# Kernel tuning notes

Hardware: AMD Instinct MI355X
Metric: run time of the kernel (lower is better)

Reference implementation:

```python
import jax, jax.numpy as jnp
import numpy as np

N = 100_000      # num_nodes
E = 1_600_000    # num directed edges (avg degree 16)
F_IN = 64
F_OUT = 64
ALPHA = 0.5      # args.alphaDir (requires_grad=False)
BETA = 0.5       # args.betaDir
GAMA = 0.5       # args.gamaDir


def setup_inputs() -> dict:
    key = jax.random.key(0)
    ks = jax.random.split(key, 16)
    s = 1.0 / np.sqrt(F_IN)  # torch Linear default init scale
    inp = {
        "x": jax.random.normal(ks[0], (N, F_IN), jnp.float32),
        "edge_index": jax.random.randint(ks[1], (2, E), 0, N, dtype=jnp.int32),
    }
    wnames = ["W_sd", "W_ds", "W0", "W1", "W2", "W3"]
    bnames = ["b_sd", "b_ds", "b0", "b1", "b2", "b3"]
    for i, (wn, bn) in enumerate(zip(wnames, bnames)):
        inp[wn] = jax.random.uniform(ks[2 + 2 * i], (F_IN, F_OUT), jnp.float32, -s, s)
        inp[bn] = jax.random.uniform(ks[3 + 2 * i], (F_OUT,), jnp.float32, -s, s)
    return inp


def reference(x, edge_index, W_sd, b_sd, W_ds, b_ds, W0, b0, W1, b1, W2, b2, W3, b3):
    row, col = edge_index[0], edge_index[1]
    seg = jax.ops.segment_sum

    # A @ v and A^T @ v as edge-list spmm (v may be [N] or [N,F])
    def Av(v):
        return seg(jnp.take(v, col, axis=0), row, num_segments=N)

    def Atv(v):
        return seg(jnp.take(v, row, axis=0), col, num_segments=N)

    ones = jnp.ones((N,), x.dtype)
    d_out = Av(ones)   # out-degrees of A (row sums)
    d_in = Atv(ones)   # in-degrees of A (col sums)

    def inv_sqrt(d):
        # d ** -0.5 with inf -> 0 (directed_norm masked_fill)
        return jnp.where(d > 0, 1.0 / jnp.sqrt(jnp.maximum(d, 1e-30)), 0.0)[:, None]

    iso, isi = inv_sqrt(d_out), inv_sqrt(d_in)

    # first-order: D_out^{-1/2} A D_in^{-1/2} @ x and its transpose counterpart
    A_x = iso * Av(isi * x)
    At_x = isi * Atv(iso * x)

    # second-order products. For M = A@A^T (symmetric): deg = A @ (A^T @ 1)
    sAAt = inv_sqrt(Av(d_in))
    AAt_x = sAAt * Av(Atv(sAAt * x))
    sAtA = inv_sqrt(Atv(d_out))
    AtA_x = sAtA * Atv(Av(sAtA * x))
    # M = A@A: out_deg = A@(A@1), in_deg = A^T@(A^T@1); A^T@A^T mirrors it
    sAAo, sAAi = inv_sqrt(Av(d_out)), inv_sqrt(Atv(d_in))
    AA_x = sAAo * Av(Av(sAAi * x))
    AtAt_x = sAAi * Atv(Atv(sAAo * x))

    def lin(h, W, b):
        return h @ W + b

    def agg(a, h0, Wa, ba, h1, Wb, bb):
        # (1+a) * (a*lin0(adj0@x) + (1-a)*lin1(adj1@x))
        return (1.0 + a) * (a * lin(h0, Wa, ba) + (1.0 - a) * lin(h1, Wb, bb))

    out = (agg(ALPHA, A_x, W_sd, b_sd, At_x, W_ds, b_ds)
           + agg(BETA, AAt_x, W0, b0, AtA_x, W1, b1)
           + agg(GAMA, AA_x, W2, b2, AtAt_x, W3, b3))
    return out
```

## Files before the change

kernel.cpp:

```cpp
#include <hip/hip_runtime.h>
#include <hip/hip_bf16.h>

typedef __hip_bfloat16 bf16;
typedef __bf16 bf16x8 __attribute__((ext_vector_type(8)));
typedef float f32x4 __attribute__((ext_vector_type(4)));
#define FDIM 64
#define KTOT 384
#define LDSK 392
#define SNIFF_THRESH 100
#define MAXNB 1024

__device__ __forceinline__ float us2f(unsigned short u) {
  union { unsigned int i; float f; } v; v.i = ((unsigned int)u) << 16; return v.f;
}
__device__ __forceinline__ unsigned short f2bu(float v) {
  bf16 h = __float2bfloat16(v);
  return *(unsigned short*)&h;
}
__device__ __forceinline__ float inv_sqrt_pos(float d) { return d > 0.f ? rsqrtf(d) : 0.f; }

__global__ __launch_bounds__(256)
void k_sniff(const unsigned short* __restrict__ xs, int n, int* __restrict__ cnt) {
  int local = 0;
  for (int i = blockIdx.x * 256 + threadIdx.x; i < n; i += 256 * 256)
    local += ((xs[i] & 0x7F80) == 0x7F80) ? 1 : 0;
  #pragma unroll
  for (int d = 32; d >= 1; d >>= 1) local += __shfl_down(local, d);
  __shared__ int sm[4];
  if ((threadIdx.x & 63) == 0) sm[threadIdx.x >> 6] = local;
  __syncthreads();
  if (threadIdx.x == 0) {
    int t = sm[0] + sm[1] + sm[2] + sm[3];
    if (t) atomicAdd(cnt, t);
  }
}

__global__ void k_convert_x(const void* __restrict__ xin, bf16* __restrict__ xb,
                            const int* __restrict__ cnt, int n) {
  int i = blockIdx.x * 256 + threadIdx.x;
  if (i >= n) return;
  if (*cnt > SNIFF_THRESH) xb[i] = __float2bfloat16(((const float*)xin)[i]);
  else                     xb[i] = ((const bf16*)xin)[i];
}

__global__ void k_convert_w(const void* W0, const void* W1, const void* W2,
                            const void* W3, const void* W4, const void* W5,
                            const void* c0, const void* c1, const void* c2,
                            const void* c3, const void* c4, const void* c5,
                            bf16* __restrict__ wt, float* __restrict__ bsum,
                            const int* __restrict__ cnt) {
  int t = blockIdx.x * 256 + threadIdx.x;
  const void* Ws[6] = {W0, W1, W2, W3, W4, W5};
  const void* Bs[6] = {c0, c1, c2, c3, c4, c5};
  bool fp = (*cnt > SNIFF_THRESH);
  if (t < 6 * 4096) {
    int si = t >> 12, o = t & 4095;
    int kk = o >> 6, n = o & 63;
    float v = fp ? ((const float*)Ws[si])[o] : __bfloat162float(((const bf16*)Ws[si])[o]);
    wt[n * KTOT + si * 64 + kk] = __float2bfloat16(v);
  } else if (t < 6 * 4096 + 64) {
    int n = t - 6 * 4096;
    float s = 0.f;
    for (int si = 0; si < 6; si++)
      s += fp ? ((const float*)Bs[si])[n] : __bfloat162float(((const bf16*)Bs[si])[n]);
    bsum[n] = s;
  }
}

__global__ __launch_bounds__(256)
void k_hist(const int* __restrict__ row, const int* __restrict__ col,
            int* __restrict__ hist, int E, int NB, int NBLK) {
  __shared__ int hr[MAXNB], hc[MAXNB];
  for (int i = threadIdx.x; i < NB; i += 256) { hr[i] = 0; hc[i] = 0; }
  __syncthreads();
  int base = blockIdx.x << 11;
  for (int k = 0; k < 8; k++) {
    int e = base + k * 256 + threadIdx.x;
    if (e < E) {
      atomicAdd(&hr[row[e] >> 7], 1);
      atomicAdd(&hc[col[e] >> 7], 1);
    }
  }
  __syncthreads();
  for (int i = threadIdx.x; i < NB; i += 256) {
    hist[(size_t)i * NBLK + blockIdx.x] = hr[i];
    hist[(size_t)(NB + i) * NBLK + blockIdx.x] = hc[i];
  }
}

__global__ void k_scan_block(const int* __restrict__ in, int* __restrict__ out,
                             int* __restrict__ part, int n) {
  __shared__ int sm[256];
  int tid = threadIdx.x;
  int i = blockIdx.x * 256 + tid;
  int v = (i < n) ? in[i] : 0;
  sm[tid] = v;
  __syncthreads();
  for (int d = 1; d < 256; d <<= 1) {
    int t = (tid >= d) ? sm[tid - d] : 0;
    __syncthreads();
    if (tid >= d) sm[tid] += t;
    __syncthreads();
  }
  if (i < n) out[i] = sm[tid] - v;
  if (tid == 255) part[blockIdx.x] = sm[255];
}

__global__ void k_scan_part(int* part, int nb) {
  __shared__ int sm[1024];
  int tid = threadIdx.x;
  int v = (tid < nb) ? part[tid] : 0;
  sm[tid] = v;
  __syncthreads();
  for (int d = 1; d < 1024; d <<= 1) {
    int t = (tid >= d) ? sm[tid - d] : 0;
    __syncthreads();
    if (tid >= d) sm[tid] += t;
    __syncthreads();
  }
  if (tid < nb) part[tid] = sm[tid] - v;
}

__global__ void k_scan_add(int* __restrict__ out, const int* __restrict__ part, int n) {
  int i = blockIdx.x * 256 + threadIdx.x;
  if (i < n) out[i] += part[blockIdx.x];
}

__global__ __launch_bounds__(256)
void k_bucket_scatter(const int* __restrict__ row, const int* __restrict__ col,
                      const int* __restrict__ hist, int* __restrict__ packed,
                      int E, int NB, int NBLK) {
  __shared__ int br[MAXNB], bc[MAXNB];
  for (int i = threadIdx.x; i < NB; i += 256) {
    br[i] = hist[(size_t)i * NBLK + blockIdx.x];
    bc[i] = hist[(size_t)(NB + i) * NBLK + blockIdx.x];
  }
  __syncthreads();
  int base = blockIdx.x << 11;
  for (int k = 0; k < 8; k++) {
    int e = base + k * 256 + threadIdx.x;
    if (e < E) {
      int r = row[e], c = col[e];
      int pr = atomicAdd(&br[r >> 7], 1);
      packed[pr] = (c << 7) | (r & 127);
      int pc = atomicAdd(&bc[c >> 7], 1);
      packed[pc] = (r << 7) | (c & 127);
    }
  }
}

__global__ __launch_bounds__(256)
void k_bucket_csr(const int* __restrict__ hist, const int* __restrict__ packed,
                  int* __restrict__ adj,
                  int* __restrict__ dout, int* __restrict__ roff,
                  int* __restrict__ din, int* __restrict__ coff,
                  int N, int NB, int NBLK, int E2) {
  __shared__ int cnt[128], scn[128], cur[128];
  int gb = blockIdx.x;
  int tid = threadIdx.x;
  if (tid < 128) { cnt[tid] = 0; cur[tid] = 0; }
  __syncthreads();
  int start = hist[(size_t)gb * NBLK];
  int end = (gb + 1 < gridDim.x) ? hist[(size_t)(gb + 1) * NBLK] : E2;
  for (int i = start + tid; i < end; i += 256)
    atomicAdd(&cnt[packed[i] & 127], 1);
  __syncthreads();
  if (tid == 0) {
    int a = 0;
    for (int i = 0; i < 128; i++) { scn[i] = a; a += cnt[i]; }
  }
  __syncthreads();
  if (tid < 128) {
    int b = gb < NB ? gb : gb - NB;
    int node = (b << 7) + tid;
    if (node < N) {
      if (gb < NB) { dout[node] = cnt[tid]; roff[node] = start + scn[tid]; }
      else         { din[node]  = cnt[tid]; coff[node] = start + scn[tid]; }
    }
  }
  __syncthreads();
  for (int i = start + tid; i < end; i += 256) {
    int v = packed[i];
    int l = v & 127, o = v >> 7;
    int rk = atomicAdd(&cur[l], 1);
    adj[start + scn[l] + rk] = o;
  }
}

__global__ __launch_bounds__(256)
void k_m4scales(const int* __restrict__ roff, const int* __restrict__ coff,
                const int* __restrict__ dout, const int* __restrict__ din,
                const int* __restrict__ adj,
                float* __restrict__ iso, float* __restrict__ isi,
                float* __restrict__ sAAt, float* __restrict__ sAtA,
                float* __restrict__ sAAo, float* __restrict__ sAAi, int N) {
  int n = blockIdx.x * 256 + threadIdx.x;
  if (n >= N) return;
  int dn = dout[n], cn = din[n];
  int o0 = roff[n];
  float aat = 0.f, aao = 0.f;
  for (int e = 0; e < dn; e++) {
    int c = adj[o0 + e];
    aat += (float)din[c];
    aao += (float)dout[c];
  }
  int i0 = coff[n];
  float ata = 0.f, aai = 0.f;
  for (int e = 0; e < cn; e++) {
    int r = adj[i0 + e];
    ata += (float)dout[r];
    aai += (float)din[r];
  }
  iso[n]  = inv_sqrt_pos((float)dn);
  isi[n]  = inv_sqrt_pos((float)cn);
  sAAt[n] = inv_sqrt_pos(aat);
  sAtA[n] = inv_sqrt_pos(ata);
  sAAo[n] = inv_sqrt_pos(aao);
  sAAi[n] = inv_sqrt_pos(aai);
}

__global__ __launch_bounds__(256)
void k_pass3(const int* __restrict__ off, const int* __restrict__ deg,
             const int* __restrict__ adj, const bf16* __restrict__ x,
             const float* __restrict__ s0, const float* __restrict__ s1,
             const float* __restrict__ s2, const float* __restrict__ wsA,
             bf16* __restrict__ outA, bf16* __restrict__ outB, bf16* __restrict__ outC,
             int N) {
  int wid = (blockIdx.x * 256 + threadIdx.x) >> 6;
  if (wid >= N) return;
  int lane = threadIdx.x & 63;
  int q = lane >> 4, t4 = (lane & 15) << 2;
  int o = off[wid], d = deg[wid];
  float a0[4] = {0,0,0,0}, a1[4] = {0,0,0,0}, a2[4] = {0,0,0,0};
  for (int e = q; e < d; e += 4) {
    int nb = adj[o + e];
    ushort4 r = *(const ushort4*)(x + (size_t)nb * FDIM + t4);
    float f0 = us2f(r.x), f1 = us2f(r.y), f2 = us2f(r.z), f3 = us2f(r.w);
    float w0 = s0[nb], w1 = s1[nb], w2 = s2[nb];
    a0[0] += w0 * f0; a0[1] += w0 * f1; a0[2] += w0 * f2; a0[3] += w0 * f3;
    a1[0] += w1 * f0; a1[1] += w1 * f1; a1[2] += w1 * f2; a1[3] += w1 * f3;
    a2[0] += w2 * f0; a2[1] += w2 * f1; a2[2] += w2 * f2; a2[3] += w2 * f3;
  }
  #pragma unroll
  for (int i = 0; i < 4; i++) {
    a0[i] += __shfl_xor(a0[i], 16); a0[i] += __shfl_xor(a0[i], 32);
    a1[i] += __shfl_xor(a1[i], 16); a1[i] += __shfl_xor(a1[i], 32);
    a2[i] += __shfl_xor(a2[i], 16); a2[i] += __shfl_xor(a2[i], 32);
  }
  if (q == 0) {
    float wA = wsA[wid];
    ushort4 uA, uB, uC;
    uA.x = f2bu(a0[0]*wA); uA.y = f2bu(a0[1]*wA); uA.z = f2bu(a0[2]*wA); uA.w = f2bu(a0[3]*wA);
    uB.x = f2bu(a1[0]);    uB.y = f2bu(a1[1]);    uB.z = f2bu(a1[2]);    uB.w = f2bu(a1[3]);
    uC.x = f2bu(a2[0]);    uC.y = f2bu(a2[1]);    uC.z = f2bu(a2[2]);    uC.w = f2bu(a2[3]);
    *(ushort4*)(outA + (size_t)wid * KTOT + t4) = uA;
    *(ushort4*)(outB + (size_t)wid * KTOT + t4) = uB;
    *(ushort4*)(outC + (size_t)wid * FDIM + t4) = uC;
  }
}

__global__ __launch_bounds__(256)
void k_pass2(const int* __restrict__ off, const int* __restrict__ deg,
             const int* __restrict__ adj,
             const bf16* __restrict__ inA, const bf16* __restrict__ inB, int strideIn,
             const float* __restrict__ wsA, const float* __restrict__ wsB,
             bf16* __restrict__ outA, bf16* __restrict__ outB, int N) {
  int wid = (blockIdx.x * 256 + threadIdx.x) >> 6;
  if (wid >= N) return;
  int lane = threadIdx.x & 63;
  int q = lane >> 4, t4 = (lane & 15) << 2;
  int o = off[wid], d = deg[wid];
  float a0[4] = {0,0,0,0}, a1[4] = {0,0,0,0};
  for (int e = q; e < d; e += 4) {
    int nb = adj[o + e];
    ushort4 rA = *(const ushort4*)(inA + (size_t)nb * strideIn + t4);
    ushort4 rB = *(const ushort4*)(inB + (size_t)nb * strideIn + t4);
    a0[0] += us2f(rA.x); a0[1] += us2f(rA.y); a0[2] += us2f(rA.z); a0[3] += us2f(rA.w);
    a1[0] += us2f(rB.x); a1[1] += us2f(rB.y); a1[2] += us2f(rB.z); a1[3] += us2f(rB.w);
  }
  #pragma unroll
  for (int i = 0; i < 4; i++) {
    a0[i] += __shfl_xor(a0[i], 16); a0[i] += __shfl_xor(a0[i], 32);
    a1[i] += __shfl_xor(a1[i], 16); a1[i] += __shfl_xor(a1[i], 32);
  }
  if (q == 0) {
    float wA = wsA[wid], wB = wsB[wid];
    ushort4 uA, uB;
    uA.x = f2bu(a0[0]*wA); uA.y = f2bu(a0[1]*wA); uA.z = f2bu(a0[2]*wA); uA.w = f2bu(a0[3]*wA);
    uB.x = f2bu(a1[0]*wB); uB.y = f2bu(a1[1]*wB); uB.z = f2bu(a1[2]*wB); uB.w = f2bu(a1[3]*wB);
    *(ushort4*)(outA + (size_t)wid * KTOT + t4) = uA;
    *(ushort4*)(outB + (size_t)wid * KTOT + t4) = uB;
  }
}

__global__ __launch_bounds__(256)
void k_final(const bf16* __restrict__ H, const bf16* __restrict__ wt,
             const float* __restrict__ bsum, void* __restrict__ outv,
             const int* __restrict__ cnt, int N) {
  __shared__ bf16 Wl[64 * LDSK];
  {
    const unsigned int* wtu = (const unsigned int*)wt;
    unsigned int* wlu = (unsigned int*)Wl;
    for (int i = threadIdx.x; i < 64 * (KTOT / 2); i += 256) {
      int n = i / (KTOT / 2), k2 = i % (KTOT / 2);
      wlu[n * (LDSK / 2) + k2] = wtu[i];
    }
  }
  __syncthreads();

  int wave = threadIdx.x >> 6, lane = threadIdx.x & 63;
  int m0 = blockIdx.x * 64 + wave * 16;
  int ml = lane & 15, kq = lane >> 4;
  const bf16* Hrow = H + (size_t)(m0 + ml) * KTOT + kq * 8;

  f32x4 acc[4] = {{0,0,0,0},{0,0,0,0},{0,0,0,0},{0,0,0,0}};
  #pragma unroll
  for (int kb = 0; kb < KTOT / 32; kb++) {
    bf16x8 a = *(const bf16x8*)(Hrow + kb * 32);
    #pragma unroll
    for (int ct = 0; ct < 4; ct++) {
      bf16x8 b = *(const bf16x8*)(Wl + (size_t)(ct * 16 + ml) * LDSK + kb * 32 + kq * 8);
      acc[ct] = __builtin_amdgcn_mfma_f32_16x16x32_bf16(a, b, acc[ct], 0, 0, 0);
    }
  }

  bool fp = (*cnt > SNIFF_THRESH);
  #pragma unroll
  for (int ct = 0; ct < 4; ct++) {
    int col = ct * 16 + ml;
    float bias = bsum[col];
    #pragma unroll
    for (int r = 0; r < 4; r++) {
      int m = m0 + kq * 4 + r;
      if (m < N) {
        float val = 0.75f * (acc[ct][r] + bias);
        if (fp) ((float*)outv)[(size_t)m * FDIM + col] = val;
        else    ((bf16*)outv)[(size_t)m * FDIM + col] = __float2bfloat16(val);
      }
    }
  }
}

extern "C" void kernel_launch(void* const* d_in, const int* in_sizes, int n_in,
                              void* d_out, int out_size, void* d_ws, size_t ws_size,
                              hipStream_t stream) {
  const void* x = d_in[0];
  const int* ei = (const int*)d_in[1];
  int NX = in_sizes[0];
  int N = NX / FDIM;
  int E = in_sizes[1] / 2;
  const int* row = ei;
  const int* col = ei + E;

  char* p = (char*)d_ws;
  auto alloc = [&](size_t bytes) {
    bytes = (bytes + 255) & ~(size_t)255;
    char* r = p; p += bytes; return r;
  };

  int*   cnt    = (int*)alloc(4);
  int*   dout_i = (int*)alloc((size_t)N * 4);
  int*   din_i  = (int*)alloc((size_t)N * 4);
  int* roff  = (int*)alloc((size_t)N * 4);
  int* coff  = (int*)alloc((size_t)N * 4);
  int* p1    = (int*)alloc(8192 * 4);
  int* p2    = (int*)alloc(1024 * 4);
  float* iso  = (float*)alloc((size_t)N * 4);
  float* isi  = (float*)alloc((size_t)N * 4);
  float* sAAt = (float*)alloc((size_t)N * 4);
  float* sAtA = (float*)alloc((size_t)N * 4);
  float* sAAo = (float*)alloc((size_t)N * 4);
  float* sAAi = (float*)alloc((size_t)N * 4);
  int* adj   = (int*)alloc((size_t)2 * E * 4);
  bf16* xb   = (bf16*)alloc((size_t)NX * 2);
  bf16* wt   = (bf16*)alloc((size_t)6 * 4096 * 2);
  float* bsum = (float*)alloc(64 * 4);
  bf16* H  = (bf16*)alloc((size_t)N * KTOT * 2);
  bf16* TQ = (bf16*)alloc((size_t)N * FDIM * 2);
  bf16* TR = (bf16*)alloc((size_t)N * FDIM * 2);

  int* hist   = (int*)TQ;
  int* packed = (int*)H;

  hipMemsetAsync(d_ws, 0, 256, stream);

  int gX = (NX + 255) / 256;
  int gN = (N + 255) / 256;
  int gW = (N + 3) / 4;
  int gF = (N + 63) / 64;

  int NB   = (N + 127) >> 7;
  int NBLK = (E + 2047) >> 11;
  int lenH = 2 * NB * NBLK;
  int g0 = (lenH + 255) / 256;
  int g1 = (g0 + 255) / 256;

  int nSniff = NX < (1 << 20) ? NX : (1 << 20);
  k_sniff<<<256, 256, 0, stream>>>((const unsigned short*)x, nSniff, cnt);
  k_convert_x<<<gX, 256, 0, stream>>>(x, xb, cnt, NX);
  k_convert_w<<<98, 256, 0, stream>>>(d_in[2], d_in[4], d_in[6], d_in[8], d_in[10], d_in[12],
                                      d_in[3], d_in[5], d_in[7], d_in[9], d_in[11], d_in[13],
                                      wt, bsum, cnt);

  k_hist<<<NBLK, 256, 0, stream>>>(row, col, hist, E, NB, NBLK);
  k_scan_block<<<g0, 256, 0, stream>>>(hist, hist, p1, lenH);
  k_scan_block<<<g1, 256, 0, stream>>>(p1, p1, p2, g0);
  k_scan_part<<<1, 1024, 0, stream>>>(p2, g1);
  k_scan_add<<<g1, 256, 0, stream>>>(p1, p2, g0);
  k_scan_add<<<g0, 256, 0, stream>>>(hist, p1, lenH);
  k_bucket_scatter<<<NBLK, 256, 0, stream>>>(row, col, hist, packed, E, NB, NBLK);
  k_bucket_csr<<<2 * NB, 256, 0, stream>>>(hist, packed, adj,
                                           dout_i, roff, din_i, coff,
                                           N, NB, NBLK, 2 * E);
  k_m4scales<<<gN, 256, 0, stream>>>(roff, coff, dout_i, din_i, adj,
                                     iso, isi, sAAt, sAtA, sAAo, sAAi, N);

  k_pass3<<<gW, 256, 0, stream>>>(roff, dout_i, adj, xb, isi, sAAi, sAtA, iso,
                                  H + 0 * 64, H + 5 * 64, TQ, N);
  k_pass3<<<gW, 256, 0, stream>>>(coff, din_i, adj, xb, iso, sAAt, sAAo, isi,
                                  H + 1 * 64, H + 3 * 64, TR, N);
  k_pass2<<<gW, 256, 0, stream>>>(roff, dout_i, adj, H + 3 * 64, H + 5 * 64, KTOT,
                                  sAAt, sAAo, H + 2 * 64, H + 4 * 64, N);
  k_pass2<<<gW, 256, 0, stream>>>(coff, din_i, adj, TQ, TR, FDIM,
                                  sAtA, sAAi, H + 3 * 64, H + 5 * 64, N);

  k_final<<<gF, 256, 0, stream>>>(H, wt, bsum, d_out, cnt, N);
}
```

Measured before the change: 573.1 us.

## Pack degrees and scales into vector structs and merge SpMM passes by direction

Degrees are stored as int2 and the six per-node scale vectors as two float4 arrays, so each neighbor lookup does one vector load instead of several scalar gathers. The two first-hop passes and the two second-hop passes are each merged into a single launch that splits blocks by direction. Intermediate results go to 128-wide packed QR buffers, so a second-hop gather reads one 16-byte vector per lane instead of two strided 8-byte loads. This cuts launch count and gather transactions, at the cost of more index arithmetic and larger scale arrays.

Measured after the change: 548.7 us. -4.3%, faster.

```diff
diff --git a/kernel.cpp b/kernel.cpp
--- a/kernel.cpp
+++ b/kernel.cpp
@@ -16,6 +16,9 @@
 __device__ __forceinline__ unsigned short f2bu(float v) {
   bf16 h = __float2bfloat16(v);
   return *(unsigned short*)&h;
+}
+__device__ __forceinline__ unsigned int pack2(float a, float b) {
+  return (unsigned int)f2bu(a) | ((unsigned int)f2bu(b) << 16);
 }
 __device__ __forceinline__ float inv_sqrt_pos(float d) { return d > 0.f ? rsqrtf(d) : 0.f; }
 
@@ -151,9 +154,8 @@
 
 __global__ __launch_bounds__(256)
 void k_bucket_csr(const int* __restrict__ hist, const int* __restrict__ packed,
-                  int* __restrict__ adj,
-                  int* __restrict__ dout, int* __restrict__ roff,
-                  int* __restrict__ din, int* __restrict__ coff,
+                  int* __restrict__ adj, int2* __restrict__ deg2,
+                  int* __restrict__ roff, int* __restrict__ coff,
                   int N, int NB, int NBLK, int E2) {
   __shared__ int cnt[128], scn[128], cur[128];
   int gb = blockIdx.x;
@@ -174,8 +176,8 @@
     int b = gb < NB ? gb : gb - NB;
     int node = (b << 7) + tid;
     if (node < N) {
-      if (gb < NB) { dout[node] = cnt[tid]; roff[node] = start + scn[tid]; }
-      else         { din[node]  = cnt[tid]; coff[node] = start + scn[tid]; }
+      if (gb < NB) { deg2[node].x = cnt[tid]; roff[node] = start + scn[tid]; }
+      else         { deg2[node].y = cnt[tid]; coff[node] = start + scn[tid]; }
     }
   }
   __syncthreads();
@@ -189,57 +191,57 @@
 
 __global__ __launch_bounds__(256)
 void k_m4scales(const int* __restrict__ roff, const int* __restrict__ coff,
-                const int* __restrict__ dout, const int* __restrict__ din,
-                const int* __restrict__ adj,
-                float* __restrict__ iso, float* __restrict__ isi,
-                float* __restrict__ sAAt, float* __restrict__ sAtA,
-                float* __restrict__ sAAo, float* __restrict__ sAAi, int N) {
+                const int2* __restrict__ deg2, const int* __restrict__ adj,
+                float4* __restrict__ sclG1, float4* __restrict__ sclG2, int N) {
   int n = blockIdx.x * 256 + threadIdx.x;
   if (n >= N) return;
-  int dn = dout[n], cn = din[n];
+  int2 dn = deg2[n];
   int o0 = roff[n];
   float aat = 0.f, aao = 0.f;
-  for (int e = 0; e < dn; e++) {
-    int c = adj[o0 + e];
-    aat += (float)din[c];
-    aao += (float)dout[c];
+  for (int e = 0; e < dn.x; e++) {
+    int2 dc = deg2[adj[o0 + e]];
+    aat += (float)dc.y;
+    aao += (float)dc.x;
   }
   int i0 = coff[n];
   float ata = 0.f, aai = 0.f;
-  for (int e = 0; e < cn; e++) {
-    int r = adj[i0 + e];
-    ata += (float)dout[r];
-    aai += (float)din[r];
-  }
-  iso[n]  = inv_sqrt_pos((float)dn);
-  isi[n]  = inv_sqrt_pos((float)cn);
-  sAAt[n] = inv_sqrt_pos(aat);
-  sAtA[n] = inv_sqrt_pos(ata);
-  sAAo[n] = inv_sqrt_pos(aao);
-  sAAi[n] = inv_sqrt_pos(aai);
-}
-
-__global__ __launch_bounds__(256)
-void k_pass3(const int* __restrict__ off, const int* __restrict__ deg,
-             const int* __restrict__ adj, const bf16* __restrict__ x,
-             const float* __restrict__ s0, const float* __restrict__ s1,
-             const float* __restrict__ s2, const float* __restrict__ wsA,
-             bf16* __restrict__ outA, bf16* __restrict__ outB, bf16* __restrict__ outC,
-             int N) {
-  int wid = (blockIdx.x * 256 + threadIdx.x) >> 6;
+  for (int e = 0; e < dn.y; e++) {
+    int2 dr = deg2[adj[i0 + e]];
+    ata += (float)dr.x;
+    aai += (float)dr.y;
+  }
+  float iso = inv_sqrt_pos((float)dn.x), isi = inv_sqrt_pos((float)dn.y);
+  sclG1[n] = make_float4(isi, inv_sqrt_pos(ata), inv_sqrt_pos(aai), iso);
+  sclG2[n] = make_float4(iso, inv_sqrt_pos(aat), inv_sqrt_pos(aao), isi);
+}
+
+__global__ __launch_bounds__(256)
+void k_passAB(const int* __restrict__ roff, const int* __restrict__ coff,
+              const int2* __restrict__ deg2, const int* __restrict__ adj,
+              const bf16* __restrict__ xb,
+              const float4* __restrict__ sclG1, const float4* __restrict__ sclG2,
+              bf16* __restrict__ H, bf16* __restrict__ QR1, bf16* __restrict__ QR2,
+              int N, int gW) {
+  int side = (blockIdx.x >= gW);
+  int lb = side ? blockIdx.x - gW : blockIdx.x;
+  int wid = (lb * 256 + (int)threadIdx.x) >> 6;
   if (wid >= N) return;
   int lane = threadIdx.x & 63;
   int q = lane >> 4, t4 = (lane & 15) << 2;
-  int o = off[wid], d = deg[wid];
+  int o, d; const float4* sclG; bf16 *outP, *outOwn, *outOth;
+  if (!side) { o = roff[wid]; d = deg2[wid].x; sclG = sclG1;
+               outP = H + 0 * 64; outOwn = QR2; outOth = QR1; }
+  else       { o = coff[wid]; d = deg2[wid].y; sclG = sclG2;
+               outP = H + 1 * 64; outOwn = QR1; outOth = QR2; }
   float a0[4] = {0,0,0,0}, a1[4] = {0,0,0,0}, a2[4] = {0,0,0,0};
   for (int e = q; e < d; e += 4) {
     int nb = adj[o + e];
-    ushort4 r = *(const ushort4*)(x + (size_t)nb * FDIM + t4);
+    ushort4 r = *(const ushort4*)(xb + (size_t)nb * FDIM + t4);
+    float4 s = sclG[nb];
     float f0 = us2f(r.x), f1 = us2f(r.y), f2 = us2f(r.z), f3 = us2f(r.w);
-    float w0 = s0[nb], w1 = s1[nb], w2 = s2[nb];
-    a0[0] += w0 * f0; a0[1] += w0 * f1; a0[2] += w0 * f2; a0[3] += w0 * f3;
-    a1[0] += w1 * f0; a1[1] += w1 * f1; a1[2] += w1 * f2; a1[3] += w1 * f3;
-    a2[0] += w2 * f0; a2[1] += w2 * f1; a2[2] += w2 * f2; a2[3] += w2 * f3;
+    a0[0] += s.x * f0; a0[1] += s.x * f1; a0[2] += s.x * f2; a0[3] += s.x * f3;
+    a1[0] += s.y * f0; a1[1] += s.y * f1; a1[2] += s.y * f2; a1[3] += s.y * f3;
+    a2[0] += s.z * f0; a2[1] += s.z * f1; a2[2] += s.z * f2; a2[3] += s.z * f3;
   }
   #pragma unroll
   for (int i = 0; i < 4; i++) {
@@ -248,48 +250,57 @@
     a2[i] += __shfl_xor(a2[i], 16); a2[i] += __shfl_xor(a2[i], 32);
   }
   if (q == 0) {
-    float wA = wsA[wid];
-    ushort4 uA, uB, uC;
-    uA.x = f2bu(a0[0]*wA); uA.y = f2bu(a0[1]*wA); uA.z = f2bu(a0[2]*wA); uA.w = f2bu(a0[3]*wA);
-    uB.x = f2bu(a1[0]);    uB.y = f2bu(a1[1]);    uB.z = f2bu(a1[2]);    uB.w = f2bu(a1[3]);
-    uC.x = f2bu(a2[0]);    uC.y = f2bu(a2[1]);    uC.z = f2bu(a2[2]);    uC.w = f2bu(a2[3]);
-    *(ushort4*)(outA + (size_t)wid * KTOT + t4) = uA;
-    *(ushort4*)(outB + (size_t)wid * KTOT + t4) = uB;
-    *(ushort4*)(outC + (size_t)wid * FDIM + t4) = uC;
-  }
-}
-
-__global__ __launch_bounds__(256)
-void k_pass2(const int* __restrict__ off, const int* __restrict__ deg,
-             const int* __restrict__ adj,
-             const bf16* __restrict__ inA, const bf16* __restrict__ inB, int strideIn,
-             const float* __restrict__ wsA, const float* __restrict__ wsB,
-             bf16* __restrict__ outA, bf16* __restrict__ outB, int N) {
-  int wid = (blockIdx.x * 256 + threadIdx.x) >> 6;
+    float w = sclG[wid].w;
+    ushort4 uP, uQ, uR;
+    uP.x = f2bu(a0[0]*w); uP.y = f2bu(a0[1]*w); uP.z = f2bu(a0[2]*w); uP.w = f2bu(a0[3]*w);
+    uQ.x = f2bu(a1[0]);   uQ.y = f2bu(a1[1]);   uQ.z = f2bu(a1[2]);   uQ.w = f2bu(a1[3]);
+    uR.x = f2bu(a2[0]);   uR.y = f2bu(a2[1]);   uR.z = f2bu(a2[2]);   uR.w = f2bu(a2[3]);
+    *(ushort4*)(outP + (size_t)wid * KTOT + t4) = uP;
+    *(ushort4*)(outOwn + (size_t)wid * 128 + t4) = uQ;
+    *(ushort4*)(outOth + (size_t)wid * 128 + 64 + t4) = uR;
+  }
+}
+
+__global__ __launch_bounds__(256)
+void k_passCD(const int* __restrict__ roff, const int* __restrict__ coff,
+              const int2* __restrict__ deg2, const int* __restrict__ adj,
+              const bf16* __restrict__ QR1, const bf16* __restrict__ QR2,
+              const float4* __restrict__ sclG1, const float4* __restrict__ sclG2,
+              bf16* __restrict__ H, int N, int gW) {
+  int side = (blockIdx.x >= gW);
+  int lb = side ? blockIdx.x - gW : blockIdx.x;
+  int wid = (lb * 256 + (int)threadIdx.x) >> 6;
   if (wid >= N) return;
   int lane = threadIdx.x & 63;
-  int q = lane >> 4, t4 = (lane & 15) << 2;
-  int o = off[wid], d = deg[wid];
-  float a0[4] = {0,0,0,0}, a1[4] = {0,0,0,0};
+  int q = lane >> 4, t = lane & 15;
+  int o, d; const bf16* QR;
+  if (!side) { o = roff[wid]; d = deg2[wid].x; QR = QR1; }
+  else       { o = coff[wid]; d = deg2[wid].y; QR = QR2; }
+  float acc[8] = {0,0,0,0,0,0,0,0};
   for (int e = q; e < d; e += 4) {
     int nb = adj[o + e];
-    ushort4 rA = *(const ushort4*)(inA + (size_t)nb * strideIn + t4);
-    ushort4 rB = *(const ushort4*)(inB + (size_t)nb * strideIn + t4);
-    a0[0] += us2f(rA.x); a0[1] += us2f(rA.y); a0[2] += us2f(rA.z); a0[3] += us2f(rA.w);
-    a1[0] += us2f(rB.x); a1[1] += us2f(rB.y); a1[2] += us2f(rB.z); a1[3] += us2f(rB.w);
+    uint4 v = *(const uint4*)(QR + (size_t)nb * 128 + t * 8);
+    acc[0] += us2f(v.x & 0xffff); acc[1] += us2f(v.x >> 16);
+    acc[2] += us2f(v.y & 0xffff); acc[3] += us2f(v.y >> 16);
+    acc[4] += us2f(v.z & 0xffff); acc[5] += us2f(v.z >> 16);
+    acc[6] += us2f(v.w & 0xffff); acc[7] += us2f(v.w >> 16);
   }
   #pragma unroll
-  for (int i = 0; i < 4; i++) {
-    a0[i] += __shfl_xor(a0[i], 16); a0[i] += __shfl_xor(a0[i], 32);
-    a1[i] += __shfl_xor(a1[i], 16); a1[i] += __shfl_xor(a1[i], 32);
+  for (int i = 0; i < 8; i++) {
+    acc[i] += __shfl_xor(acc[i], 16);
+    acc[i] += __shfl_xor(acc[i], 32);
   }
   if (q == 0) {
-    float wA = wsA[wid], wB = wsB[wid];
-    ushort4 uA, uB;
-    uA.x = f2bu(a0[0]*wA); uA.y = f2bu(a0[1]*wA); uA.z = f2bu(a0[2]*wA); uA.w = f2bu(a0[3]*wA);
-    uB.x = f2bu(a1[0]*wB); uB.y = f2bu(a1[1]*wB); uB.z = f2bu(a1[2]*wB); uB.w = f2bu(a1[3]*wB);
-    *(ushort4*)(outA + (size_t)wid * KTOT + t4) = uA;
-    *(ushort4*)(outB + (size_t)wid * KTOT + t4) = uB;
+    float4 s = side ? sclG1[wid] : sclG2[wid];
+    float ws = (t < 8) ? s.y : s.z;
+    int slot = side ? (t < 8 ? 3 : 5) : (t < 8 ? 2 : 4);
+    int col = slot * 64 + (t & 7) * 8;
+    uint4 ov;
+    ov.x = pack2(acc[0]*ws, acc[1]*ws);
+    ov.y = pack2(acc[2]*ws, acc[3]*ws);
+    ov.z = pack2(acc[4]*ws, acc[5]*ws);
+    ov.w = pack2(acc[6]*ws, acc[7]*ws);
+    *(uint4*)(H + (size_t)wid * KTOT + col) = ov;
   }
 }
 
@@ -358,28 +369,23 @@
     char* r = p; p += bytes; return r;
   };
 
-  int*   cnt    = (int*)alloc(4);
-  int*   dout_i = (int*)alloc((size_t)N * 4);
-  int*   din_i  = (int*)alloc((size_t)N * 4);
-  int* roff  = (int*)alloc((size_t)N * 4);
-  int* coff  = (int*)alloc((size_t)N * 4);
-  int* p1    = (int*)alloc(8192 * 4);
-  int* p2    = (int*)alloc(1024 * 4);
-  float* iso  = (float*)alloc((size_t)N * 4);
-  float* isi  = (float*)alloc((size_t)N * 4);
-  float* sAAt = (float*)alloc((size_t)N * 4);
-  float* sAtA = (float*)alloc((size_t)N * 4);
-  float* sAAo = (float*)alloc((size_t)N * 4);
-  float* sAAi = (float*)alloc((size_t)N * 4);
-  int* adj   = (int*)alloc((size_t)2 * E * 4);
-  bf16* xb   = (bf16*)alloc((size_t)NX * 2);
-  bf16* wt   = (bf16*)alloc((size_t)6 * 4096 * 2);
+  int*   cnt  = (int*)alloc(4);
+  int2*  deg2 = (int2*)alloc((size_t)N * 8);
+  int* roff   = (int*)alloc((size_t)N * 4);
+  int* coff   = (int*)alloc((size_t)N * 4);
+  int* p1     = (int*)alloc(8192 * 4);
+  int* p2     = (int*)alloc(1024 * 4);
+  float4* sclG1 = (float4*)alloc((size_t)N * 16);
+  float4* sclG2 = (float4*)alloc((size_t)N * 16);
+  int* adj    = (int*)alloc((size_t)2 * E * 4);
+  bf16* xb    = (bf16*)alloc((size_t)NX * 2);
+  bf16* wt    = (bf16*)alloc((size_t)6 * 4096 * 2);
   float* bsum = (float*)alloc(64 * 4);
-  bf16* H  = (bf16*)alloc((size_t)N * KTOT * 2);
-  bf16* TQ = (bf16*)alloc((size_t)N * FDIM * 2);
-  bf16* TR = (bf16*)alloc((size_t)N * FDIM * 2);
-
-  int* hist   = (int*)TQ;
+  bf16* H   = (bf16*)alloc((size_t)N * KTOT * 2);
+  bf16* QR1 = (bf16*)alloc((size_t)N * 128 * 2);
+  bf16* QR2 = (bf16*)alloc((size_t)N * 128 * 2);
+
+  int* hist   = (int*)QR1;
   int* packed = (int*)H;
 
   hipMemsetAsync(d_ws, 0, 256, stream);
@@ -409,20 +415,14 @@
   k_scan_add<<<g1, 256, 0, stream>>>(p1, p2, g0);
   k_scan_add<<<g0, 256, 0, stream>>>(hist, p1, lenH);
   k_bucket_scatter<<<NBLK, 256, 0, stream>>>(row, col, hist, packed, E, NB, NBLK);
-  k_bucket_csr<<<2 * NB, 256, 0, stream>>>(hist, packed, adj,
-                                           dout_i, roff, din_i, coff,
+  k_bucket_csr<<<2 * NB, 256, 0, stream>>>(hist, packed, adj, deg2, roff, coff,
                                            N, NB, NBLK, 2 * E);
-  k_m4scales<<<gN, 256, 0, stream>>>(roff, coff, dout_i, din_i, adj,
-                                     iso, isi, sAAt, sAtA, sAAo, sAAi, N);
-
-  k_pass3<<<gW, 256, 0, stream>>>(roff, dout_i, adj, xb, isi, sAAi, sAtA, iso,
-                                  H + 0 * 64, H + 5 * 64, TQ, N);
-  k_pass3<<<gW, 256, 0, stream>>>(coff, din_i, adj, xb, iso, sAAt, sAAo, isi,
-                                  H + 1 * 64, H + 3 * 64, TR, N);
-  k_pass2<<<gW, 256, 0, stream>>>(roff, dout_i, adj, H + 3 * 64, H + 5 * 64, KTOT,
-                                  sAAt, sAAo, H + 2 * 64, H + 4 * 64, N);
-  k_pass2<<<gW, 256, 0, stream>>>(coff, din_i, adj, TQ, TR, FDIM,
-                                  sAtA, sAAi, H + 3 * 64, H + 5 * 64, N);
+  k_m4scales<<<gN, 256, 0, stream>>>(roff, coff, deg2, adj, sclG1, sclG2, N);
+
+  k_passAB<<<2 * gW, 256, 0, stream>>>(roff, coff, deg2, adj, xb, sclG1, sclG2,
+                                       H, QR1, QR2, N, gW);
+  k_passCD<<<2 * gW, 256, 0, stream>>>(roff, coff, deg2, adj, QR1, QR2, sclG1, sclG2,
+                                       H, N, gW);
 
   k_final<<<gF, 256, 0, stream>>>(H, wt, bsum, d_out, cnt, N);
 }
```
